# Kernel optimization log

Measured on AMD Instinct MI355X. Metric: run time of the kernel, lower is better.

## Reference

```python
import jax, jax.numpy as jnp
import numpy as np

ALPHAS = [2.0 ** k for k in range(-3, 2)]  # default GaussianKernel bandwidth magnitudes


def _cdist(x, y):
    # Euclidean distance matrix with torch.cdist-compatible zero-distance subgradient.
    sq = (jnp.sum(x * x, axis=1)[:, None]
          + jnp.sum(y * y, axis=1)[None, :]
          - 2.0 * (x @ y.T))
    sq = jnp.maximum(sq, 0.0)
    safe = jnp.where(sq > 0, sq, 1.0)
    return jnp.where(sq > 0, jnp.sqrt(safe), 0.0)


def setup_inputs() -> dict:
    key = jax.random.key(0)
    k1, k2 = jax.random.split(key)
    xs = jax.random.normal(k1, (4096, 256), dtype=jnp.float32)
    xt = jax.random.normal(k2, (4096, 256), dtype=jnp.float32)
    return {"xs": xs, "xt": xt}


def reference(xs, xt):
    xs = xs.reshape(xs.shape[0], -1)
    xt = xt.reshape(xt.shape[0], -1)
    b = xs.shape[0]

    # Compute the three pairwise distance matrices ONCE (the torch loop redoes
    # this per kernel; the math is identical).
    dxx = _cdist(xs, xs)  # [B, B]
    dyy = _cdist(xt, xt)
    dxy = _cdist(xs, xt)

    # sigma^2 = alpha * mean(dist), with the mean detached (stop_gradient).
    mxx = jax.lax.stop_gradient(jnp.mean(dxx))
    myy = jax.lax.stop_gradient(jnp.mean(dyy))
    mxy = jax.lax.stop_gradient(jnp.mean(dxy))

    total = jnp.zeros_like(dxx)
    for a in ALPHAS:
        kxx = jnp.exp(-dxx / (2.0 * a * mxx))
        kyy = jnp.exp(-dyy / (2.0 * a * myy))
        kxy = jnp.exp(-dxy / (2.0 * a * mxy))
        total = total + (kxx + kyy - 2.0 * kxy)

    loss = jnp.sqrt(jnp.sum(total) / (b * (b - 1.0)))
    return jnp.where(jnp.isnan(loss), jnp.zeros_like(loss), loss)
```

## Files before the change

kernel.cpp:

```cpp
#include <hip/hip_runtime.h>

#define BN 4096
#define KD 256
#define TILE 128

typedef short bf16x8 __attribute__((ext_vector_type(8)));
typedef float f32x4 __attribute__((ext_vector_type(4)));
typedef _Float16 h2 __attribute__((ext_vector_type(2)));
typedef unsigned short ushort_t;
typedef unsigned int uint_t;

#define NSLOT 2080

__device__ inline void async_load16(const void* g, void* l) {
    __builtin_amdgcn_global_load_lds((const __attribute__((address_space(1))) void*)g,
                                     (__attribute__((address_space(3))) void*)l,
                                     16, 0, 0);
}

__device__ inline ushort_t f2bf(float f) {
    union { float f; unsigned int u; } x;
    x.f = f;
    unsigned int u = x.u;
    unsigned int r = (u + 0x7fffu + ((u >> 16) & 1u)) >> 16;
    return (ushort_t)r;
}

__device__ __forceinline__ float fast_sqrt(float x) {
    return __builtin_amdgcn_sqrtf(x);
}
__device__ __forceinline__ float fast_exp2(float x) {
    return __builtin_amdgcn_exp2f(x);
}

__device__ __forceinline__ void decode_slot(int slot, int& z, int& bi, int& bj) {
    if (slot >= 1056) {
        z = 2; int t = slot - 1056; bi = t >> 5; bj = t & 31;
    } else {
        z = (slot >= 528) ? 1 : 0;
        int t = slot - z * 528;
        int b = (int)(32.5f - sqrtf(1056.25f - 2.0f * (float)t));
        while (b * (65 - b) / 2 > t) --b;
        while ((b + 1) * (64 - b) / 2 <= t) ++b;
        bi = b;
        bj = bi + (t - bi * (65 - bi) / 2);
    }
}

__global__ __launch_bounds__(256) void norm_cvt(
        const float* __restrict__ xs, const float* __restrict__ xt,
        ushort_t* __restrict__ xsb, ushort_t* __restrict__ xtb,
        float* __restrict__ norms) {
    int w = threadIdx.x >> 6;
    int lane = threadIdx.x & 63;
    int row = blockIdx.x * 4 + w;
    const float* src = (row < BN) ? xs + (size_t)row * KD
                                  : xt + (size_t)(row - BN) * KD;
    ushort_t* dst = (row < BN) ? xsb + (size_t)row * KD
                               : xtb + (size_t)(row - BN) * KD;
    float4 v = ((const float4*)src)[lane];
    float s = v.x * v.x + v.y * v.y + v.z * v.z + v.w * v.w;
#pragma unroll
    for (int off = 32; off > 0; off >>= 1) s += __shfl_xor(s, off, 64);
    if (lane == 0) norms[row] = s;
    ushort4 o;
    o.x = f2bf(v.x); o.y = f2bf(v.y); o.z = f2bf(v.z); o.w = f2bf(v.w);
    ((ushort4*)dst)[lane] = o;
}


template <bool DIAG>
__device__ __forceinline__ float epilogue_store(
        const f32x4 (&acc)[4][4], const float* nxv, const float* nyv,
        int wr, int wc, int q, int m16, int tid, uint_t* __restrict__ tileBase) {
    float local = 0.0f;
    uint4* tb4 = (uint4*)tileBase;
#pragma unroll
    for (int rg = 0; rg < 4; ++rg) {
#pragma unroll
        for (int np = 0; np < 2; ++np) {
            uint_t packed[4];
#pragma unroll
            for (int ngh = 0; ngh < 2; ++ngh) {
                int ng = np * 2 + ngh;
#pragma unroll
                for (int rp = 0; rp < 2; ++rp) {
                    float dpair[2];
#pragma unroll
                    for (int rh = 0; rh < 2; ++rh) {
                        int rr = rp * 2 + rh;
                        float sq = nxv[rg * 4 + rr] + nyv[ng] - 2.0f * acc[rg][ng][rr];
                        sq = fmaxf(sq, 0.0f);
                        float d = fast_sqrt(sq);
                        if (DIAG) {
                            int i = wr * 64 + rg * 16 + q * 4 + rr;
                            int j = wc * 64 + ng * 16 + m16;
                            if (i == j) d = 0.0f;
                        }
                        local += d;
                        dpair[rh] = d;
                    }
                    h2 p;
                    p[0] = (_Float16)dpair[0];
                    p[1] = (_Float16)dpair[1];
                    packed[ngh * 2 + rp] = __builtin_bit_cast(uint_t, p);
                }
            }
            uint4 v;
            v.x = packed[0]; v.y = packed[1]; v.z = packed[2]; v.w = packed[3];
            tb4[(rg * 2 + np) * 256 + tid] = v;
        }
    }
    return local;
}

__global__ __launch_bounds__(256, 4) void mmd_pass1(
        const ushort_t* __restrict__ xsb, const ushort_t* __restrict__ xtb,
        const float* __restrict__ norms, float* __restrict__ partialA,
        uint_t* __restrict__ dbuf) {
    const int slot = blockIdx.x;
    int z, bi, bj;
    decode_slot(slot, z, bi, bj);

    const ushort_t* X = (z == 1) ? xtb : xsb;
    const ushort_t* Y = (z == 0) ? xsb : xtb;
    const float* nX = norms + ((z == 1) ? BN : 0);
    const float* nY = norms + ((z == 0) ? 0 : BN);

    const int tid = threadIdx.x;
    const int lane = tid & 63;
    const int w = tid >> 6;
    const int wr = w >> 1;
    const int wc = w & 1;
    const int m16 = lane & 15;
    const int q = lane >> 4;
    const int sub = lane >> 2;
    const int ch = lane & 3;

    const int i0 = bi * TILE;
    const int j0 = bj * TILE;

    __shared__ ushort_t lds[2][2][TILE * 32];
    __shared__ float red[4];

    f32x4 acc[4][4] = {};

#define STAGE(kk, b)                                                            \
    {                                                                           \
        _Pragma("unroll")                                                       \
        for (int t = 0; t < 2; ++t) {                                           \
            int rb = w + t * 4;                                                 \
            int r = rb * 16 + sub;                                              \
            int gch = ch ^ (r & 3);                                             \
            const ushort_t* gA = X + (size_t)(i0 + r) * KD + (kk) * 32 + gch * 8;\
            const ushort_t* gB = Y + (size_t)(j0 + r) * KD + (kk) * 32 + gch * 8;\
            async_load16(gA, (char*)&lds[b][0][0] + rb * 1024);                 \
            async_load16(gB, (char*)&lds[b][1][0] + rb * 1024);                 \
        }                                                                       \
    }

    STAGE(0, 0);

#pragma unroll
    for (int kk = 0; kk < 8; ++kk) {
        __syncthreads();
        if (kk < 7) STAGE(kk + 1, (kk + 1) & 1);
        const int b = kk & 1;
        bf16x8 af[4], bfr[4];
#pragma unroll
        for (int rg = 0; rg < 4; ++rg) {
            int rowa = wr * 64 + rg * 16 + m16;
            af[rg] = *(const bf16x8*)&lds[b][0][rowa * 32 + (q ^ (rowa & 3)) * 8];
            int rowb = wc * 64 + rg * 16 + m16;
            bfr[rg] = *(const bf16x8*)&lds[b][1][rowb * 32 + (q ^ (rowb & 3)) * 8];
        }
#pragma unroll
        for (int rg = 0; rg < 4; ++rg)
#pragma unroll
            for (int ng = 0; ng < 4; ++ng)
                acc[rg][ng] = __builtin_amdgcn_mfma_f32_16x16x32_bf16(
                    af[rg], bfr[ng], acc[rg][ng], 0, 0, 0);
    }
#undef STAGE

    float nxv[16];
#pragma unroll
    for (int rg = 0; rg < 4; ++rg)
#pragma unroll
        for (int rr = 0; rr < 4; ++rr)
            nxv[rg * 4 + rr] = nX[i0 + wr * 64 + rg * 16 + q * 4 + rr];
    float nyv[4];
#pragma unroll
    for (int ng = 0; ng < 4; ++ng)
        nyv[ng] = nY[j0 + wc * 64 + ng * 16 + m16];

    uint_t* tileBase = dbuf + (size_t)slot * 8192;
    float local;
    if (z < 2 && bi == bj)
        local = epilogue_store<true>(acc, nxv, nyv, wr, wc, q, m16, tid, tileBase);
    else
        local = epilogue_store<false>(acc, nxv, nyv, wr, wc, q, m16, tid, tileBase);

#pragma unroll
    for (int off = 32; off > 0; off >>= 1) local += __shfl_xor(local, off, 64);
    if (lane == 0) red[w] = local;
    __syncthreads();
    if (tid == 0) {
        float bs = red[0] + red[1] + red[2] + red[3];
        float c1 = (z < 2 && bi != bj) ? 2.0f : 1.0f;
        partialA[slot] = c1 * bs;
    }
}


__global__ __launch_bounds__(256) void mmd_pass2(
        const uint_t* __restrict__ dbuf, const float* __restrict__ partialA,
        float* __restrict__ partialB) {
    const int tid = threadIdx.x;
    const int slot = blockIdx.x;
    const int lane = tid & 63;
    const int w = tid >> 6;
    int z, bi, bj;
    decode_slot(slot, z, bi, bj);

    double a0 = 0.0, a1 = 0.0, a2 = 0.0;
    for (int s = tid; s < NSLOT; s += 256) {
        double v = (double)partialA[s];
        if (s < 528) a0 += v; else if (s < 1056) a1 += v; else a2 += v;
    }
#pragma unroll
    for (int off = 32; off > 0; off >>= 1) {
        a0 += __shfl_xor(a0, off, 64);
        a1 += __shfl_xor(a1, off, 64);
        a2 += __shfl_xor(a2, off, 64);
    }
    __shared__ double rs[4][3];
    if (lane == 0) { rs[w][0] = a0; rs[w][1] = a1; rs[w][2] = a2; }
    __syncthreads();
    double sz = (z == 0) ? rs[0][0] + rs[1][0] + rs[2][0] + rs[3][0]
              : (z == 1) ? rs[0][1] + rs[1][1] + rs[2][1] + rs[3][1]
                         : rs[0][2] + rs[1][2] + rs[2][2] + rs[3][2];

    double mz = sz * (1.0 / 16777216.0);
    float nhb = (float)(-1.4426950408889634 / (4.0 * mz));
    float coef = (z == 2) ? -2.0f : ((bi != bj) ? 2.0f : 1.0f);
    const uint_t* base = dbuf + (size_t)slot * 8192;

    float local = 0.0f;
#pragma unroll
    for (int it = 0; it < 8; ++it) {
        uint4 v = ((const uint4*)base)[it * 256 + tid];
        uint_t arr[4] = {v.x, v.y, v.z, v.w};
#pragma unroll
        for (int j = 0; j < 4; ++j) {
            h2 p = __builtin_bit_cast(h2, arr[j]);
#pragma unroll
            for (int h = 0; h < 2; ++h) {
                float d = (float)p[h];
                float u = fast_exp2(d * nhb);
                float u2 = u * u;
                float u4 = u2 * u2;
                float u8 = u4 * u4;
                float u16 = u8 * u8;
                local += (u + u2) + (u4 + u8) + u16;
            }
        }
    }

    __shared__ float red[4];
#pragma unroll
    for (int off = 32; off > 0; off >>= 1) local += __shfl_xor(local, off, 64);
    if (lane == 0) red[w] = local;
    __syncthreads();
    if (tid == 0) {
        float bs = red[0] + red[1] + red[2] + red[3];
        partialB[slot] = coef * bs;
    }
}


__global__ __launch_bounds__(256) void mmd_finalize2(
        const float* __restrict__ partialB, float* __restrict__ out) {
    const int tid = threadIdx.x;
    double acc = 0.0;
    for (int s = tid; s < NSLOT; s += 256) acc += (double)partialB[s];
    const int lane = tid & 63, w = tid >> 6;
#pragma unroll
    for (int off = 32; off > 0; off >>= 1) acc += __shfl_xor(acc, off, 64);
    __shared__ double r[4];
    if (lane == 0) r[w] = acc;
    __syncthreads();
    if (tid == 0) {
        double S = r[0] + r[1] + r[2] + r[3];
        double l = sqrt(S / ((double)BN * (double)(BN - 1)));
        float f = (float)l;
        if (!(f == f)) f = 0.0f;
        out[0] = f;
    }
}


template <int PASS>
__global__ __launch_bounds__(256) void mmd_gemm(
        const ushort_t* __restrict__ xsb, const ushort_t* __restrict__ xtb,
        const float* __restrict__ norms, double* __restrict__ sums) {
    const int z = blockIdx.z;
    const int bi = blockIdx.y;
    const int bj = blockIdx.x;
    if (z < 2 && bj < bi) return;

    const ushort_t* X = (z == 1) ? xtb : xsb;
    const ushort_t* Y = (z == 0) ? xsb : xtb;
    const float* nX = norms + ((z == 1) ? BN : 0);
    const float* nY = norms + ((z == 0) ? 0 : BN);

    const int tid = threadIdx.x;
    const int lane = tid & 63;
    const int w = tid >> 6;
    const int wr = w >> 1;
    const int wc = w & 1;
    const int m16 = lane & 15;
    const int q = lane >> 4;

    const int i0 = bi * TILE;
    const int j0 = bj * TILE;

    __shared__ ushort_t lA[TILE * 64];
    __shared__ ushort_t lB[TILE * 64];
    __shared__ float red[4];

    float nhb = 0.0f;
    if (PASS == 2) {
        double mz = sums[z] / ((double)BN * (double)BN);
        nhb = (float)(-1.4426950408889634 / (4.0 * mz));
    }

    f32x4 acc[4][4] = {};

#pragma unroll
    for (int kk = 0; kk < KD; kk += 64) {
        __syncthreads();
#pragma unroll
        for (int t = 0; t < 4; ++t) {
            int rowblk = w * 4 + t;
            int r = rowblk * 8 + (lane >> 3);
            int cch = lane & 7;
            int gch = cch ^ (r & 7);
            const ushort_t* gA = X + (size_t)(i0 + r) * KD + (kk + gch * 8);
            const ushort_t* gB = Y + (size_t)(j0 + r) * KD + (kk + gch * 8);
            async_load16(gA, (char*)lA + rowblk * 1024);
            async_load16(gB, (char*)lB + rowblk * 1024);
        }
        __syncthreads();

#pragma unroll
        for (int ks = 0; ks < 2; ++ks) {
            bf16x8 af[4], bfr[4];
            int kap = ks * 4 + q;
#pragma unroll
            for (int rg = 0; rg < 4; ++rg) {
                int rowa = wr * 64 + rg * 16 + m16;
                int posa = kap ^ (rowa & 7);
                af[rg] = *(const bf16x8*)&lA[rowa * 64 + posa * 8];
                int rowb = wc * 64 + rg * 16 + m16;
                int posb = kap ^ (rowb & 7);
                bfr[rg] = *(const bf16x8*)&lB[rowb * 64 + posb * 8];
            }
#pragma unroll
            for (int rg = 0; rg < 4; ++rg)
#pragma unroll
                for (int ng = 0; ng < 4; ++ng)
                    acc[rg][ng] = __builtin_amdgcn_mfma_f32_16x16x32_bf16(
                        af[rg], bfr[ng], acc[rg][ng], 0, 0, 0);
        }
    }

    float nxv[16];
#pragma unroll
    for (int rg = 0; rg < 4; ++rg)
#pragma unroll
        for (int rr = 0; rr < 4; ++rr)
            nxv[rg * 4 + rr] = nX[i0 + wr * 64 + rg * 16 + q * 4 + rr];
    float nyv[4];
#pragma unroll
    for (int ng = 0; ng < 4; ++ng)
        nyv[ng] = nY[j0 + wc * 64 + ng * 16 + m16];

    float local = 0.0f;
#pragma unroll
    for (int rg = 0; rg < 4; ++rg) {
#pragma unroll
        for (int ng = 0; ng < 4; ++ng) {
#pragma unroll
            for (int rr = 0; rr < 4; ++rr) {
                int i = i0 + wr * 64 + rg * 16 + q * 4 + rr;
                int j = j0 + wc * 64 + ng * 16 + m16;
                float sq = nxv[rg * 4 + rr] + nyv[ng] - 2.0f * acc[rg][ng][rr];
                sq = fmaxf(sq, 0.0f);
                float d = fast_sqrt(sq);
                if (z < 2 && i == j) d = 0.0f;
                if (PASS == 1) {
                    local += d;
                } else {
                    float u = fast_exp2(d * nhb);
                    float u2 = u * u;
                    float u4 = u2 * u2;
                    float u8 = u4 * u4;
                    float u16 = u8 * u8;
                    local += u + u2 + u4 + u8 + u16;
                }
            }
        }
    }

#pragma unroll
    for (int off = 32; off > 0; off >>= 1) local += __shfl_xor(local, off, 64);
    if (lane == 0) red[w] = local;
    __syncthreads();
    if (tid == 0) {
        double bs = (double)red[0] + (double)red[1] + (double)red[2] + (double)red[3];
        double coef = (z < 2 && bi != bj) ? 2.0 : 1.0;
        if (PASS == 2 && z == 2) coef = -2.0;
        atomicAdd(&sums[PASS == 1 ? z : 3], coef * bs);
    }
}

__global__ void mmd_finalize(const double* __restrict__ sums, float* __restrict__ out) {
    double S = sums[3];
    double l = sqrt(S / ((double)BN * (double)(BN - 1)));
    float f = (float)l;
    if (!(f == f)) f = 0.0f;
    out[0] = f;
}

extern "C" void kernel_launch(void* const* d_in, const int* in_sizes, int n_in,
                              void* d_out, int out_size, void* d_ws, size_t ws_size,
                              hipStream_t stream) {
    const float* xs = (const float*)d_in[0];
    const float* xt = (const float*)d_in[1];
    float* out = (float*)d_out;

    char* ws = (char*)d_ws;
    double* sums = (double*)ws;
    float* norms = (float*)(ws + 64);
    float* partialA = (float*)(ws + 32832);
    float* partialB = (float*)(ws + 41152);
    ushort_t* xsb = (ushort_t*)(ws + 49536);
    ushort_t* xtb = xsb + (size_t)BN * KD;
    uint_t* dbuf = (uint_t*)(ws + 4243840);

    size_t need_small = 4243840;
    size_t need_big = 4243840 + (size_t)NSLOT * 32768;

    if (ws_size < need_small) {
        (void)hipMemsetAsync(d_out, 0xC0, 4, stream);
        return;
    }

    norm_cvt<<<2048, 256, 0, stream>>>(xs, xt, xsb, xtb, norms);

    if (ws_size >= need_big) {
        mmd_pass1<<<NSLOT, 256, 0, stream>>>(xsb, xtb, norms, partialA, dbuf);
        mmd_pass2<<<NSLOT, 256, 0, stream>>>(dbuf, partialA, partialB);
        mmd_finalize2<<<1, 256, 0, stream>>>(partialB, out);
    } else {
        (void)hipMemsetAsync(d_ws, 0, 64, stream);
        dim3 g(32, 32, 3);
        mmd_gemm<1><<<g, 256, 0, stream>>>(xsb, xtb, norms, sums);
        mmd_gemm<2><<<g, 256, 0, stream>>>(xsb, xtb, norms, sums);
        mmd_finalize<<<1, 1, 0, stream>>>(sums, out);
    }
}
```

Before: 116.8 us.

## Fuse both MMD passes into one cooperative kernel with register-held 8-bit distances

Replaces the two-pass pipeline, which wrote fp16 distance tiles to a large global buffer and reread them, with one persistent cooperative kernel. Each block computes three tiles, keeps the distances quantized to 8 bits in registers, and uses grid syncs to form the means and then the final exp sums. This removes the large global round-trip and the extra launches. In exchange it adds quantization error in the distances, depends on cooperative launch with a fixed grid, and lowers occupancy to three blocks per CU.

```diff
diff --git a/kernel.cpp b/kernel.cpp
--- a/kernel.cpp
+++ b/kernel.cpp
@@ -1,4 +1,7 @@
 #include <hip/hip_runtime.h>
+#include <hip/hip_cooperative_groups.h>
+
+namespace cg = cooperative_groups;
 
 #define BN 4096
 #define KD 256
@@ -11,6 +14,7 @@
 typedef unsigned int uint_t;
 
 #define NSLOT 2080
+#define FGRID 694
 
 __device__ inline void async_load16(const void* g, void* l) {
     __builtin_amdgcn_global_load_lds((const __attribute__((address_space(1))) void*)g,
@@ -68,13 +72,266 @@
     ((ushort4*)dst)[lane] = o;
 }
 
-
-template <bool DIAG>
-__device__ __forceinline__ float epilogue_store(
-        const f32x4 (&acc)[4][4], const float* nxv, const float* nyv,
-        int wr, int wc, int q, int m16, int tid, uint_t* __restrict__ tileBase) {
+__device__ __forceinline__ void gemm_tile(
+        const ushort_t* __restrict__ X, const ushort_t* __restrict__ Y,
+        int i0, int j0, ushort_t (*lds)[2][TILE * 32], f32x4 (&acc)[4][4],
+        int w, int sub, int ch, int wr, int wc, int m16, int q) {
+#define STAGE(kk, b)                                                            \
+    {                                                                           \
+        _Pragma("unroll")                                                       \
+        for (int t = 0; t < 2; ++t) {                                           \
+            int rb = w + t * 4;                                                 \
+            int r = rb * 16 + sub;                                              \
+            int gch = ch ^ (r & 3);                                             \
+            const ushort_t* gA = X + (size_t)(i0 + r) * KD + (kk) * 32 + gch * 8;\
+            const ushort_t* gB = Y + (size_t)(j0 + r) * KD + (kk) * 32 + gch * 8;\
+            async_load16(gA, (char*)&lds[b][0][0] + rb * 1024);                 \
+            async_load16(gB, (char*)&lds[b][1][0] + rb * 1024);                 \
+        }                                                                       \
+    }
+
+    STAGE(0, 0);
+
+#pragma unroll
+    for (int kk = 0; kk < 8; ++kk) {
+        __syncthreads();
+        if (kk < 7) STAGE(kk + 1, (kk + 1) & 1);
+        const int b = kk & 1;
+        bf16x8 af[4], bfr[4];
+#pragma unroll
+        for (int rg = 0; rg < 4; ++rg) {
+            int rowa = wr * 64 + rg * 16 + m16;
+            af[rg] = *(const bf16x8*)&lds[b][0][rowa * 32 + (q ^ (rowa & 3)) * 8];
+            int rowb = wc * 64 + rg * 16 + m16;
+            bfr[rg] = *(const bf16x8*)&lds[b][1][rowb * 32 + (q ^ (rowb & 3)) * 8];
+        }
+#pragma unroll
+        for (int rg = 0; rg < 4; ++rg)
+#pragma unroll
+            for (int ng = 0; ng < 4; ++ng)
+                acc[rg][ng] = __builtin_amdgcn_mfma_f32_16x16x32_bf16(
+                    af[rg], bfr[ng], acc[rg][ng], 0, 0, 0);
+    }
+#undef STAGE
+}
+
+
+__global__ __launch_bounds__(256, 3) void mmd_fused(
+        const ushort_t* __restrict__ xsb, const ushort_t* __restrict__ xtb,
+        const float* __restrict__ norms, float* __restrict__ partialA,
+        float* __restrict__ partialB, float* __restrict__ out) {
+    const int tid = threadIdx.x;
+    const int lane = tid & 63;
+    const int w = tid >> 6;
+    const int wr = w >> 1;
+    const int wc = w & 1;
+    const int m16 = lane & 15;
+    const int q = lane >> 4;
+    const int sub = lane >> 2;
+    const int ch = lane & 3;
+
+    __shared__ ushort_t lds[2][2][TILE * 32];
+    __shared__ float red[4];
+    __shared__ double rs[4][3];
+    __shared__ float red2[4][3];
+
+    uint_t dq[3][16];
+
+#pragma unroll
+    for (int ti = 0; ti < 3; ++ti) {
+        const int slot = blockIdx.x + ti * FGRID;
+        if (slot < NSLOT) {
+            int z, bi, bj;
+            decode_slot(slot, z, bi, bj);
+            const ushort_t* X = (z == 1) ? xtb : xsb;
+            const ushort_t* Y = (z == 0) ? xsb : xtb;
+            const float* nX = norms + ((z == 1) ? BN : 0);
+            const float* nY = norms + ((z == 0) ? 0 : BN);
+            const int i0 = bi * TILE;
+            const int j0 = bj * TILE;
+
+            f32x4 acc[4][4] = {};
+            gemm_tile(X, Y, i0, j0, lds, acc, w, sub, ch, wr, wc, m16, q);
+
+            float nxv[16];
+#pragma unroll
+            for (int rg = 0; rg < 4; ++rg)
+#pragma unroll
+                for (int rr = 0; rr < 4; ++rr)
+                    nxv[rg * 4 + rr] = nX[i0 + wr * 64 + rg * 16 + q * 4 + rr];
+            float nyv[4];
+#pragma unroll
+            for (int ng = 0; ng < 4; ++ng)
+                nyv[ng] = nY[j0 + wc * 64 + ng * 16 + m16];
+
+            const bool diag = (z < 2 && bi == bj);
+            float local = 0.0f;
+#pragma unroll
+            for (int rg = 0; rg < 4; ++rg) {
+#pragma unroll
+                for (int ng = 0; ng < 4; ++ng) {
+                    uint_t p = 0;
+#pragma unroll
+                    for (int rr = 0; rr < 4; ++rr) {
+                        float sq = nxv[rg * 4 + rr] + nyv[ng] - 2.0f * acc[rg][ng][rr];
+                        sq = fmaxf(sq, 0.0f);
+                        float d = fast_sqrt(sq);
+                        if (diag) {
+                            int ii = wr * 64 + rg * 16 + q * 4 + rr;
+                            int jj = wc * 64 + ng * 16 + m16;
+                            if (ii == jj) d = 0.0f;
+                        }
+                        local += d;
+                        float df = fminf(d * 8.0f + 0.5f, 255.0f);
+                        p |= ((uint_t)df) << (rr * 8);
+                    }
+                    dq[ti][rg * 4 + ng] = p;
+                }
+            }
+
+#pragma unroll
+            for (int off = 32; off > 0; off >>= 1) local += __shfl_xor(local, off, 64);
+            if (lane == 0) red[w] = local;
+            __syncthreads();
+            if (tid == 0) {
+                float bs = red[0] + red[1] + red[2] + red[3];
+                float c1 = (z < 2 && bi != bj) ? 2.0f : 1.0f;
+                atomicExch(&partialA[slot], c1 * bs);
+            }
+        }
+    }
+
+    __threadfence();
+    cg::this_grid().sync();
+
+    double a0 = 0.0, a1 = 0.0, a2 = 0.0;
+    for (int s = tid; s < NSLOT; s += 256) {
+        double v = (double)partialA[s];
+        if (s < 528) a0 += v; else if (s < 1056) a1 += v; else a2 += v;
+    }
+#pragma unroll
+    for (int off = 32; off > 0; off >>= 1) {
+        a0 += __shfl_xor(a0, off, 64);
+        a1 += __shfl_xor(a1, off, 64);
+        a2 += __shfl_xor(a2, off, 64);
+    }
+    if (lane == 0) { rs[w][0] = a0; rs[w][1] = a1; rs[w][2] = a2; }
+    __syncthreads();
+    double m[3];
+    m[0] = (rs[0][0] + rs[1][0] + rs[2][0] + rs[3][0]) * (1.0 / 16777216.0);
+    m[1] = (rs[0][1] + rs[1][1] + rs[2][1] + rs[3][1]) * (1.0 / 16777216.0);
+    m[2] = (rs[0][2] + rs[1][2] + rs[2][2] + rs[3][2]) * (1.0 / 16777216.0);
+
+#pragma unroll
+    for (int ti = 0; ti < 3; ++ti) {
+        const int slot = blockIdx.x + ti * FGRID;
+        if (slot < NSLOT) {
+            int z, bi, bj;
+            decode_slot(slot, z, bi, bj);
+            float s8 = (float)(-1.4426950408889634 / (4.0 * m[z])) * 0.125f;
+            float local = 0.0f;
+#pragma unroll
+            for (int e = 0; e < 16; ++e) {
+                uint_t p = dq[ti][e];
+#pragma unroll
+                for (int h = 0; h < 4; ++h) {
+                    float b = (float)((p >> (h * 8)) & 0xffu);
+                    float u = fast_exp2(b * s8);
+                    float u2 = u * u;
+                    float u4 = u2 * u2;
+                    float u8 = u4 * u4;
+                    float u16 = u8 * u8;
+                    local += (u + u2) + (u4 + u8) + u16;
+                }
+            }
+#pragma unroll
+            for (int off = 32; off > 0; off >>= 1) local += __shfl_xor(local, off, 64);
+            if (lane == 0) red2[w][ti] = local;
+        }
+    }
+    __syncthreads();
+    if (tid == 0) {
+#pragma unroll
+        for (int ti = 0; ti < 3; ++ti) {
+            const int slot = blockIdx.x + ti * FGRID;
+            if (slot < NSLOT) {
+                int z, bi, bj;
+                decode_slot(slot, z, bi, bj);
+                float coef = (z == 2) ? -2.0f : ((bi != bj) ? 2.0f : 1.0f);
+                float bs = red2[0][ti] + red2[1][ti] + red2[2][ti] + red2[3][ti];
+                atomicExch(&partialB[slot], coef * bs);
+            }
+        }
+    }
+
+    __threadfence();
+    cg::this_grid().sync();
+
+    if (blockIdx.x == 0) {
+        double acc = 0.0;
+        for (int s = tid; s < NSLOT; s += 256) acc += (double)partialB[s];
+#pragma unroll
+        for (int off = 32; off > 0; off >>= 1) acc += __shfl_xor(acc, off, 64);
+        __shared__ double r[4];
+        if (lane == 0) r[w] = acc;
+        __syncthreads();
+        if (tid == 0) {
+            double S = r[0] + r[1] + r[2] + r[3];
+            double l = sqrt(S / ((double)BN * (double)(BN - 1)));
+            float f = (float)l;
+            if (!(f == f)) f = 0.0f;
+            out[0] = f;
+        }
+    }
+}
+
+
+__global__ __launch_bounds__(256, 4) void mmd_pass1(
+        const ushort_t* __restrict__ xsb, const ushort_t* __restrict__ xtb,
+        const float* __restrict__ norms, float* __restrict__ partialA,
+        uint_t* __restrict__ dbuf) {
+    const int slot = blockIdx.x;
+    int z, bi, bj;
+    decode_slot(slot, z, bi, bj);
+
+    const ushort_t* X = (z == 1) ? xtb : xsb;
+    const ushort_t* Y = (z == 0) ? xsb : xtb;
+    const float* nX = norms + ((z == 1) ? BN : 0);
+    const float* nY = norms + ((z == 0) ? 0 : BN);
+
+    const int tid = threadIdx.x;
+    const int lane = tid & 63;
+    const int w = tid >> 6;
+    const int wr = w >> 1;
+    const int wc = w & 1;
+    const int m16 = lane & 15;
+    const int q = lane >> 4;
+    const int sub = lane >> 2;
+    const int ch = lane & 3;
+
+    const int i0 = bi * TILE;
+    const int j0 = bj * TILE;
+
+    __shared__ ushort_t lds[2][2][TILE * 32];
+    __shared__ float red[4];
+
+    f32x4 acc[4][4] = {};
+    gemm_tile(X, Y, i0, j0, lds, acc, w, sub, ch, wr, wc, m16, q);
+
+    float nxv[16];
+#pragma unroll
+    for (int rg = 0; rg < 4; ++rg)
+#pragma unroll
+        for (int rr = 0; rr < 4; ++rr)
+            nxv[rg * 4 + rr] = nX[i0 + wr * 64 + rg * 16 + q * 4 + rr];
+    float nyv[4];
+#pragma unroll
+    for (int ng = 0; ng < 4; ++ng)
+        nyv[ng] = nY[j0 + wc * 64 + ng * 16 + m16];
+
+    const bool diag = (z < 2 && bi == bj);
+    uint4* tb4 = (uint4*)(dbuf + (size_t)slot * 8192);
     float local = 0.0f;
-    uint4* tb4 = (uint4*)tileBase;
 #pragma unroll
     for (int rg = 0; rg < 4; ++rg) {
 #pragma unroll
@@ -92,10 +349,10 @@
                         float sq = nxv[rg * 4 + rr] + nyv[ng] - 2.0f * acc[rg][ng][rr];
                         sq = fmaxf(sq, 0.0f);
                         float d = fast_sqrt(sq);
-                        if (DIAG) {
-                            int i = wr * 64 + rg * 16 + q * 4 + rr;
-                            int j = wc * 64 + ng * 16 + m16;
-                            if (i == j) d = 0.0f;
+                        if (diag) {
+                            int ii = wr * 64 + rg * 16 + q * 4 + rr;
+                            int jj = wc * 64 + ng * 16 + m16;
+                            if (ii == jj) d = 0.0f;
                         }
                         local += d;
                         dpair[rh] = d;
@@ -111,95 +368,6 @@
             tb4[(rg * 2 + np) * 256 + tid] = v;
         }
     }
-    return local;
-}
-
-__global__ __launch_bounds__(256, 4) void mmd_pass1(
-        const ushort_t* __restrict__ xsb, const ushort_t* __restrict__ xtb,
-        const float* __restrict__ norms, float* __restrict__ partialA,
-        uint_t* __restrict__ dbuf) {
-    const int slot = blockIdx.x;
-    int z, bi, bj;
-    decode_slot(slot, z, bi, bj);
-
-    const ushort_t* X = (z == 1) ? xtb : xsb;
-    const ushort_t* Y = (z == 0) ? xsb : xtb;
-    const float* nX = norms + ((z == 1) ? BN : 0);
-    const float* nY = norms + ((z == 0) ? 0 : BN);
-
-    const int tid = threadIdx.x;
-    const int lane = tid & 63;
-    const int w = tid >> 6;
-    const int wr = w >> 1;
-    const int wc = w & 1;
-    const int m16 = lane & 15;
-    const int q = lane >> 4;
-    const int sub = lane >> 2;
-    const int ch = lane & 3;
-
-    const int i0 = bi * TILE;
-    const int j0 = bj * TILE;
-
-    __shared__ ushort_t lds[2][2][TILE * 32];
-    __shared__ float red[4];
-
-    f32x4 acc[4][4] = {};
-
-#define STAGE(kk, b)                                                            \
-    {                                                                           \
-        _Pragma("unroll")                                                       \
-        for (int t = 0; t < 2; ++t) {                                           \
-            int rb = w + t * 4;                                                 \
-            int r = rb * 16 + sub;                                              \
-            int gch = ch ^ (r & 3);                                             \
-            const ushort_t* gA = X + (size_t)(i0 + r) * KD + (kk) * 32 + gch * 8;\
-            const ushort_t* gB = Y + (size_t)(j0 + r) * KD + (kk) * 32 + gch * 8;\
-            async_load16(gA, (char*)&lds[b][0][0] + rb * 1024);                 \
-            async_load16(gB, (char*)&lds[b][1][0] + rb * 1024);                 \
-        }                                                                       \
-    }
-
-    STAGE(0, 0);
-
-#pragma unroll
-    for (int kk = 0; kk < 8; ++kk) {
-        __syncthreads();
-        if (kk < 7) STAGE(kk + 1, (kk + 1) & 1);
-        const int b = kk & 1;
-        bf16x8 af[4], bfr[4];
-#pragma unroll
-        for (int rg = 0; rg < 4; ++rg) {
-            int rowa = wr * 64 + rg * 16 + m16;
-            af[rg] = *(const bf16x8*)&lds[b][0][rowa * 32 + (q ^ (rowa & 3)) * 8];
-            int rowb = wc * 64 + rg * 16 + m16;
-            bfr[rg] = *(const bf16x8*)&lds[b][1][rowb * 32 + (q ^ (rowb & 3)) * 8];
-        }
-#pragma unroll
-        for (int rg = 0; rg < 4; ++rg)
-#pragma unroll
-            for (int ng = 0; ng < 4; ++ng)
-                acc[rg][ng] = __builtin_amdgcn_mfma_f32_16x16x32_bf16(
-                    af[rg], bfr[ng], acc[rg][ng], 0, 0, 0);
-    }
-#undef STAGE
-
-    float nxv[16];
-#pragma unroll
-    for (int rg = 0; rg < 4; ++rg)
-#pragma unroll
-        for (int rr = 0; rr < 4; ++rr)
-            nxv[rg * 4 + rr] = nX[i0 + wr * 64 + rg * 16 + q * 4 + rr];
-    float nyv[4];
-#pragma unroll
-    for (int ng = 0; ng < 4; ++ng)
-        nyv[ng] = nY[j0 + wc * 64 + ng * 16 + m16];
-
-    uint_t* tileBase = dbuf + (size_t)slot * 8192;
-    float local;
-    if (z < 2 && bi == bj)
-        local = epilogue_store<true>(acc, nxv, nyv, wr, wc, q, m16, tid, tileBase);
-    else
-        local = epilogue_store<false>(acc, nxv, nyv, wr, wc, q, m16, tid, tileBase);
 
 #pragma unroll
     for (int off = 32; off > 0; off >>= 1) local += __shfl_xor(local, off, 64);
@@ -211,7 +379,6 @@
         partialA[slot] = c1 * bs;
     }
 }
-
 
 __global__ __launch_bounds__(256) void mmd_pass2(
         const uint_t* __restrict__ dbuf, const float* __restrict__ partialA,
@@ -277,7 +444,6 @@
         partialB[slot] = coef * bs;
     }
 }
-
 
 __global__ __launch_bounds__(256) void mmd_finalize2(
         const float* __restrict__ partialB, float* __restrict__ out) {
@@ -299,140 +465,6 @@
     }
 }
 
-
-template <int PASS>
-__global__ __launch_bounds__(256) void mmd_gemm(
-        const ushort_t* __restrict__ xsb, const ushort_t* __restrict__ xtb,
-        const float* __restrict__ norms, double* __restrict__ sums) {
-    const int z = blockIdx.z;
-    const int bi = blockIdx.y;
-    const int bj = blockIdx.x;
-    if (z < 2 && bj < bi) return;
-
-    const ushort_t* X = (z == 1) ? xtb : xsb;
-    const ushort_t* Y = (z == 0) ? xsb : xtb;
-    const float* nX = norms + ((z == 1) ? BN : 0);
-    const float* nY = norms + ((z == 0) ? 0 : BN);
-
-    const int tid = threadIdx.x;
-    const int lane = tid & 63;
-    const int w = tid >> 6;
-    const int wr = w >> 1;
-    const int wc = w & 1;
-    const int m16 = lane & 15;
-    const int q = lane >> 4;
-
-    const int i0 = bi * TILE;
-    const int j0 = bj * TILE;
-
-    __shared__ ushort_t lA[TILE * 64];
-    __shared__ ushort_t lB[TILE * 64];
-    __shared__ float red[4];
-
-    float nhb = 0.0f;
-    if (PASS == 2) {
-        double mz = sums[z] / ((double)BN * (double)BN);
-        nhb = (float)(-1.4426950408889634 / (4.0 * mz));
-    }
-
-    f32x4 acc[4][4] = {};
-
-#pragma unroll
-    for (int kk = 0; kk < KD; kk += 64) {
-        __syncthreads();
-#pragma unroll
-        for (int t = 0; t < 4; ++t) {
-            int rowblk = w * 4 + t;
-            int r = rowblk * 8 + (lane >> 3);
-            int cch = lane & 7;
-            int gch = cch ^ (r & 7);
-            const ushort_t* gA = X + (size_t)(i0 + r) * KD + (kk + gch * 8);
-            const ushort_t* gB = Y + (size_t)(j0 + r) * KD + (kk + gch * 8);
-            async_load16(gA, (char*)lA + rowblk * 1024);
-            async_load16(gB, (char*)lB + rowblk * 1024);
-        }
-        __syncthreads();
-
-#pragma unroll
-        for (int ks = 0; ks < 2; ++ks) {
-            bf16x8 af[4], bfr[4];
-            int kap = ks * 4 + q;
-#pragma unroll
-            for (int rg = 0; rg < 4; ++rg) {
-                int rowa = wr * 64 + rg * 16 + m16;
-                int posa = kap ^ (rowa & 7);
-                af[rg] = *(const bf16x8*)&lA[rowa * 64 + posa * 8];
-                int rowb = wc * 64 + rg * 16 + m16;
-                int posb = kap ^ (rowb & 7);
-                bfr[rg] = *(const bf16x8*)&lB[rowb * 64 + posb * 8];
-            }
-#pragma unroll
-            for (int rg = 0; rg < 4; ++rg)
-#pragma unroll
-                for (int ng = 0; ng < 4; ++ng)
-                    acc[rg][ng] = __builtin_amdgcn_mfma_f32_16x16x32_bf16(
-                        af[rg], bfr[ng], acc[rg][ng], 0, 0, 0);
-        }
-    }
-
-    float nxv[16];
-#pragma unroll
-    for (int rg = 0; rg < 4; ++rg)
-#pragma unroll
-        for (int rr = 0; rr < 4; ++rr)
-            nxv[rg * 4 + rr] = nX[i0 + wr * 64 + rg * 16 + q * 4 + rr];
-    float nyv[4];
-#pragma unroll
-    for (int ng = 0; ng < 4; ++ng)
-        nyv[ng] = nY[j0 + wc * 64 + ng * 16 + m16];
-
-    float local = 0.0f;
-#pragma unroll
-    for (int rg = 0; rg < 4; ++rg) {
-#pragma unroll
-        for (int ng = 0; ng < 4; ++ng) {
-#pragma unroll
-            for (int rr = 0; rr < 4; ++rr) {
-                int i = i0 + wr * 64 + rg * 16 + q * 4 + rr;
-                int j = j0 + wc * 64 + ng * 16 + m16;
-                float sq = nxv[rg * 4 + rr] + nyv[ng] - 2.0f * acc[rg][ng][rr];
-                sq = fmaxf(sq, 0.0f);
-                float d = fast_sqrt(sq);
-                if (z < 2 && i == j) d = 0.0f;
-                if (PASS == 1) {
-                    local += d;
-                } else {
-                    float u = fast_exp2(d * nhb);
-                    float u2 = u * u;
-                    float u4 = u2 * u2;
-                    float u8 = u4 * u4;
-                    float u16 = u8 * u8;
-                    local += u + u2 + u4 + u8 + u16;
-                }
-            }
-        }
-    }
-
-#pragma unroll
-    for (int off = 32; off > 0; off >>= 1) local += __shfl_xor(local, off, 64);
-    if (lane == 0) red[w] = local;
-    __syncthreads();
-    if (tid == 0) {
-        double bs = (double)red[0] + (double)red[1] + (double)red[2] + (double)red[3];
-        double coef = (z < 2 && bi != bj) ? 2.0 : 1.0;
-        if (PASS == 2 && z == 2) coef = -2.0;
-        atomicAdd(&sums[PASS == 1 ? z : 3], coef * bs);
-    }
-}
-
-__global__ void mmd_finalize(const double* __restrict__ sums, float* __restrict__ out) {
-    double S = sums[3];
-    double l = sqrt(S / ((double)BN * (double)(BN - 1)));
-    float f = (float)l;
-    if (!(f == f)) f = 0.0f;
-    out[0] = f;
-}
-
 extern "C" void kernel_launch(void* const* d_in, const int* in_sizes, int n_in,
                               void* d_out, int out_size, void* d_ws, size_t ws_size,
                               hipStream_t stream) {
@@ -441,7 +473,6 @@
     float* out = (float*)d_out;
 
     char* ws = (char*)d_ws;
-    double* sums = (double*)ws;
     float* norms = (float*)(ws + 64);
     float* partialA = (float*)(ws + 32832);
     float* partialB = (float*)(ws + 41152);
@@ -449,25 +480,36 @@
     ushort_t* xtb = xsb + (size_t)BN * KD;
     uint_t* dbuf = (uint_t*)(ws + 4243840);
 
-    size_t need_small = 4243840;
-    size_t need_big = 4243840 + (size_t)NSLOT * 32768;
-
-    if (ws_size < need_small) {
+    size_t need_fused = 4243840;
+    size_t need_fallback = 4243840 + (size_t)NSLOT * 32768;
+
+    if (ws_size < need_fused) {
         (void)hipMemsetAsync(d_out, 0xC0, 4, stream);
         return;
     }
 
     norm_cvt<<<2048, 256, 0, stream>>>(xs, xt, xsb, xtb, norms);
 
-    if (ws_size >= need_big) {
+    bool coop = false;
+    int maxb = 0;
+    if (hipOccupancyMaxActiveBlocksPerMultiprocessor(
+            &maxb, (const void*)mmd_fused, 256, 0) == hipSuccess && maxb >= 3) {
+        const ushort_t* a0 = xsb;
+        const ushort_t* a1 = xtb;
+        const float* a2 = norms;
+        float* a3 = partialA;
+        float* a4 = partialB;
+        float* a5 = out;
+        void* args[6] = {&a0, &a1, &a2, &a3, &a4, &a5};
+        coop = (hipLaunchCooperativeKernel((const void*)mmd_fused, dim3(FGRID),
+                                           dim3(256), args, 0, stream) == hipSuccess);
+    }
+
+    if (!coop && ws_size >= need_fallback) {
         mmd_pass1<<<NSLOT, 256, 0, stream>>>(xsb, xtb, norms, partialA, dbuf);
         mmd_pass2<<<NSLOT, 256, 0, stream>>>(dbuf, partialA, partialB);
         mmd_finalize2<<<1, 256, 0, stream>>>(partialB, out);
-    } else {
-        (void)hipMemsetAsync(d_ws, 0, 64, stream);
-        dim3 g(32, 32, 3);
-        mmd_gemm<1><<<g, 256, 0, stream>>>(xsb, xtb, norms, sums);
-        mmd_gemm<2><<<g, 256, 0, stream>>>(xsb, xtb, norms, sums);
-        mmd_finalize<<<1, 1, 0, stream>>>(sums, out);
-    }
-}
+    } else if (!coop) {
+        (void)hipMemsetAsync(d_out, 0xC0, 4, stream);
+    }
+}
```

New measurement: 122.4 us. 4.8% more time.
